# Performance work log

Measured on AMD Instinct MI355X. Metric: run time of the kernel, lower is better.

The kernel has to match this reference:

```python
import jax, jax.numpy as jnp
import numpy as np

N_ROUTES = 200000
N_REGIONS = 2048
D_IN = 3
EMBED_DIM0 = 100
LSTM_DIM = 100
H1 = 1000
D_OUT = 100


def setup_inputs() -> dict:
    key = jax.random.key(0)
    ks = jax.random.split(key, 14)
    s = 0.1
    return {
        "routes_last": jax.random.normal(ks[0], (N_ROUTES, D_IN), jnp.float32),
        "route_region_ids": jax.random.randint(ks[1], (N_ROUTES,), 0, N_REGIONS),
        # linear0: Linear(3, 100)
        "W0": jax.random.normal(ks[2], (EMBED_DIM0, D_IN), jnp.float32) * s,
        "b0": jax.random.normal(ks[3], (EMBED_DIM0,), jnp.float32) * s,
        # LSTMCell(100, 100): gate order i, f, g, o
        "Wih": jax.random.normal(ks[4], (4 * LSTM_DIM, EMBED_DIM0), jnp.float32) * s,
        "bih": jax.random.normal(ks[5], (4 * LSTM_DIM,), jnp.float32) * s,
        "Whh": jax.random.normal(ks[6], (4 * LSTM_DIM, LSTM_DIM), jnp.float32) * s,
        "bhh": jax.random.normal(ks[7], (4 * LSTM_DIM,), jnp.float32) * s,
        # learned initial state (nn.Parameter rand(1, lstm_dim))
        "h0": jax.random.uniform(ks[8], (1, LSTM_DIM), jnp.float32),
        "c0": jax.random.uniform(ks[9], (1, LSTM_DIM), jnp.float32),
        # linears1: Linear(100,1000) -> ReLU -> Linear(1000,100)
        "W1": jax.random.normal(ks[10], (H1, LSTM_DIM), jnp.float32) * s,
        "b1": jax.random.normal(ks[11], (H1,), jnp.float32) * s,
        "W2": jax.random.normal(ks[12], (D_OUT, H1), jnp.float32) * s,
        "b2": jax.random.normal(ks[13], (D_OUT,), jnp.float32) * s,
        "num_regions": N_REGIONS,
    }


def reference(routes_last, route_region_ids, W0, b0, Wih, bih, Whh, bhh, h0, c0, W1, b1, W2, b2, num_regions):
    # Note: the original LSTM loop always restarts from (h0, c0) and keeps only the
    # last hx, so only the last timestep of each route matters. routes_last is that point.
    e = routes_last @ W0.T + b0                       # [N, 100]
    gates = e @ Wih.T + bih + (h0 @ Whh.T + bhh)      # [N, 400]; h0 broadcasts
    i_g, f_g, g_g, o_g = jnp.split(gates, 4, axis=-1)
    c = jax.nn.sigmoid(f_g) * c0 + jax.nn.sigmoid(i_g) * jnp.tanh(g_g)
    h = jax.nn.sigmoid(o_g) * jnp.tanh(c)             # [N, 100]
    hx = jax.nn.relu(h @ W1.T + b1) @ W2.T + b2       # [N, 100]
    # sum routes within each region (ragged sum)
    region_emb = jax.ops.segment_sum(hx, route_region_ids, num_segments=num_regions)  # [R, 100]
    region_emb = region_emb / jnp.linalg.norm(region_emb, axis=-1, keepdims=True)
    cov = region_emb @ region_emb.T                   # [R, R] cosine similarity
    idx = jnp.arange(num_regions)
    cov = cov.at[idx, idx].set(-jnp.inf)
    return cov
```

## Files before the change

### kernel.cpp

```cpp
#include <hip/hip_runtime.h>
#include <math.h>

#define NR 200000
#define NREG 2048
#define BR 128
#define NBLK 1563

typedef short bf16x8 __attribute__((ext_vector_type(8)));
typedef float f32x4 __attribute__((ext_vector_type(4)));

#define SH_WIH 410752
#define SH_W1  (SH_WIH + 57344)
#define SH_W2  (SH_W1 + 131072)
#define B_LIST 1427712
#define B_CNT  2227712
#define B_BASE 2235904
#define B_CURS 2244112
#define B_HXB  2252800
#define WS_REQ 91852800ULL

#define L_SA  0
#define L_HB  16384
#define L_SB  16384
#define L_T1  30720
#define L_XS  49152
#define L_GBP 50688
#define L_C0P 52480
#define L_B1C 52928
#define L_RID 53184
#define L_BYTES 53696

__device__ __forceinline__ unsigned f2bf(float f) {
    unsigned u = __builtin_bit_cast(unsigned, f);
    u += 0x7fff + ((u >> 16) & 1);
    return u >> 16;
}
__device__ __forceinline__ unsigned cvtpk(float lo, float hi) {
    unsigned r;
    asm("v_cvt_pk_bf16_f32 %0, %1, %2" : "=v"(r) : "v"(lo), "v"(hi));
    return r;
}
__device__ __forceinline__ float sigm(float x) { return 1.0f / (1.0f + __expf(-x)); }
__device__ __forceinline__ float tanhfast(float x) {
    float t = __expf(2.0f * fabsf(x));
    float r = 1.0f - 2.0f / (t + 1.0f);
    return copysignf(r, x);
}
__device__ __forceinline__ f32x4 mfma16(bf16x8 a, bf16x8 b, f32x4 c) {
    return __builtin_amdgcn_mfma_f32_16x16x32_bf16(a, b, c, 0, 0, 0);
}

__global__ __launch_bounds__(1024) void k_zero(float* __restrict__ p, int n) {
    int i = blockIdx.x * 1024 + threadIdx.x;
    if (i < n) p[i] = 0.0f;
}

__global__ __launch_bounds__(256) void k_hist(const int* __restrict__ ids,
                                              int* __restrict__ cnt) {
    int i = blockIdx.x * 256 + threadIdx.x;
    if (i < NR) atomicAdd(&cnt[ids[i]], 1);
}

__global__ __launch_bounds__(1024) void k_scan(const int* __restrict__ cnt,
                                               int* __restrict__ base,
                                               int* __restrict__ cursor) {
    __shared__ int sc[2048];
    const int t = threadIdx.x;
    sc[t] = cnt[t];
    sc[t + 1024] = cnt[t + 1024];
    __syncthreads();
    for (int off = 1; off < 2048; off <<= 1) {
        int v0 = (t >= off) ? sc[t - off] : 0;
        int v1 = sc[t + 1024 - off];
        __syncthreads();
        sc[t] += v0;
        sc[t + 1024] += v1;
        __syncthreads();
    }
    int b0 = (t == 0) ? 0 : sc[t - 1];
    int b1v = sc[t + 1023];
    base[t] = b0;          cursor[t] = b0;
    base[t + 1024] = b1v;  cursor[t + 1024] = b1v;
    if (t == 0) base[2048] = sc[2047];
}

__global__ __launch_bounds__(256) void k_scatter(const int* __restrict__ ids,
                                                 int* __restrict__ cursor,
                                                 int* __restrict__ list) {
    int i = blockIdx.x * 256 + threadIdx.x;
    if (i < NR) {
        int pos = atomicAdd(&cursor[ids[i]], 1);
        list[pos] = i;
    }
}

__global__ __launch_bounds__(256) void k_prep(
    const float* __restrict__ Wih, const float* __restrict__ bih,
    const float* __restrict__ bhh, const float* __restrict__ Whh,
    const float* __restrict__ h0,  const float* __restrict__ c0,
    const float* __restrict__ W1,  const float* __restrict__ W2,
    float* __restrict__ wsf, short* __restrict__ wsh)
{
    int idx = blockIdx.x * 256 + threadIdx.x;
    if (idx < 57344) {
        int st = idx >> 13, s = idx & 8191;
        int row = s >> 7, c4 = (s >> 3) & 15, e = s & 7;
        int kc = c4 ^ (row & 15);
        int k = kc * 8 + e;
        int g = row >> 4, j = st * 16 + (row & 15);
        float v = (j < 100 && k < 100) ? Wih[(g * 100 + j) * 100 + k] : 0.f;
        wsh[SH_WIH + idx] = (short)f2bf(v);
        return;
    }
    idx -= 57344;
    if (idx < 131072) {
        int st = idx >> 13, s = idx & 8191;
        int row = s >> 7, c4 = (s >> 3) & 15, e = s & 7;
        int kc = c4 ^ (row & 15);
        int k = kc * 8 + e;
        int m = st * 64 + row;
        float v = (m < 1000 && k < 100) ? W1[m * 100 + k] : 0.f;
        wsh[SH_W1 + idx] = (short)f2bf(v);
        return;
    }
    idx -= 131072;
    if (idx < 114688) {
        int st = idx / 7168, s = idx - st * 7168;
        int row = s >> 6, c4 = (s >> 3) & 7, e = s & 7;
        int kc = c4 ^ (row & 7);
        int m = st * 64 + kc * 8 + e;
        float v = (row < 100 && m < 1000) ? W2[row * 1000 + m] : 0.f;
        wsh[SH_W2 + idx] = (short)f2bf(v);
        return;
    }
    idx -= 114688;
    if (idx < 448) {
        int jt = idx >> 6, r = idx & 63, g = r >> 4, j = jt * 16 + (r & 15);
        float s = 0.f;
        if (j < 100) {
            s = bih[g * 100 + j] + bhh[g * 100 + j];
            const float* wr = &Whh[(g * 100 + j) * 100];
            for (int k = 0; k < 100; ++k) s += h0[k] * wr[k];
        }
        wsf[204800 + idx] = s;
        return;
    }
    idx -= 448;
    if (idx < 112) wsf[205248 + idx] = (idx < 100) ? c0[idx] : 0.f;
}

__global__ __launch_bounds__(256, 3) void k_routes(
    const float* __restrict__ routes, const int* __restrict__ ids,
    const float* __restrict__ W0, const float* __restrict__ b0,
    const float* __restrict__ b1, const float* __restrict__ b2,
    const float* __restrict__ wsf, const short* __restrict__ wsh,
    float* __restrict__ racc, float* __restrict__ hxb, int use_hxb)
{
    __shared__ __align__(16) float ldsf[L_BYTES / 4];
    char* L = (char*)ldsf;
    const int tid = threadIdx.x;
    const int w = tid >> 6, l = tid & 63;
    const int lr = l & 15, lg = l >> 4;
    const int rbase = blockIdx.x * BR;

    float* xs  = (float*)(L + L_XS);
    float* gbp = (float*)(L + L_GBP);
    float* c0p = (float*)(L + L_C0P);
    float* b1c = (float*)(L + L_B1C);
    int*   rid = (int*)(L + L_RID);

    if (tid < 96) {
        float4 v;
        int gi = rbase * 3 + tid * 4;
        v.x = (gi + 0 < NR * 3) ? routes[gi + 0] : 0.f;
        v.y = (gi + 1 < NR * 3) ? routes[gi + 1] : 0.f;
        v.z = (gi + 2 < NR * 3) ? routes[gi + 2] : 0.f;
        v.w = (gi + 3 < NR * 3) ? routes[gi + 3] : 0.f;
        *(float4*)(xs + tid * 4) = v;
    } else if (tid >= 128) {
        int t = tid - 128;
        rid[t] = (rbase + t < NR) ? ids[rbase + t] : 0;
    }
    for (int i = tid; i < 448; i += 256) gbp[i] = wsf[204800 + i];
    for (int i = tid; i < 112; i += 256) c0p[i] = wsf[205248 + i];
    if (tid < 128) {
        int q = tid & 15;
        f32x4 z = {0.f, 0.f, 0.f, 0.f};
        *(f32x4*)(L + L_HB + tid * 256 + ((14 ^ q) << 4)) = z;
        *(f32x4*)(L + L_HB + tid * 256 + ((15 ^ q) << 4)) = z;
    }
    __syncthreads();

    bf16x8 be[2][4];
    #pragma unroll
    for (int rt = 0; rt < 2; ++rt) {
        int rl = w * 32 + rt * 16 + lr;
        float x0 = xs[rl * 3], x1 = xs[rl * 3 + 1], x2 = xs[rl * 3 + 2];
        #pragma unroll
        for (int ks = 0; ks < 4; ++ks) {
            bf16x8 v;
            #pragma unroll
            for (int j = 0; j < 8; ++j) {
                int k = ks * 32 + lg * 8 + j;
                float e = 0.f;
                if (k < 100)
                    e = b0[k] + x0 * W0[3 * k] + x1 * W0[3 * k + 1] + x2 * W0[3 * k + 2];
                v[j] = (short)f2bf(e);
            }
            be[rt][ks] = v;
        }
    }

    const f32x4* gsrc = (const f32x4*)(wsh + SH_WIH);
    f32x4 pa[4];
    #pragma unroll
    for (int t = 0; t < 4; ++t) pa[t] = gsrc[tid + t * 256];
    #pragma unroll 1
    for (int jt = 0; jt < 7; ++jt) {
        __syncthreads();
        {
            f32x4* dst = (f32x4*)(L + L_SA);
            #pragma unroll
            for (int t = 0; t < 4; ++t) dst[tid + t * 256] = pa[t];
        }
        __syncthreads();
        if (jt < 6) {
            #pragma unroll
            for (int t = 0; t < 4; ++t) pa[t] = gsrc[(jt + 1) * 1024 + tid + t * 256];
        }
        f32x4 acc[4][2];
        #pragma unroll
        for (int g = 0; g < 4; ++g) {
            bf16x8 aw[4];
            #pragma unroll
            for (int ks = 0; ks < 4; ++ks)
                aw[ks] = *(bf16x8*)(L + L_SA + (g * 16 + lr) * 256 + (((lg + 4 * ks) ^ lr) << 4));
            #pragma unroll
            for (int rt = 0; rt < 2; ++rt) {
                f32x4 a = {0.f, 0.f, 0.f, 0.f};
                #pragma unroll
                for (int ks = 0; ks < 4; ++ks) a = mfma16(aw[ks], be[rt][ks], a);
                acc[g][rt] = a;
            }
        }
        const f32x4 gi_ = *(const f32x4*)(gbp + jt * 64 +  0 + lg * 4);
        const f32x4 gf_ = *(const f32x4*)(gbp + jt * 64 + 16 + lg * 4);
        const f32x4 gg_ = *(const f32x4*)(gbp + jt * 64 + 32 + lg * 4);
        const f32x4 go_ = *(const f32x4*)(gbp + jt * 64 + 48 + lg * 4);
        const f32x4 c0v = *(const f32x4*)(c0p + jt * 16 + lg * 4);
        #pragma unroll
        for (int rt = 0; rt < 2; ++rt) {
            int route = w * 32 + rt * 16 + lr;
            float hv[4];
            #pragma unroll
            for (int i = 0; i < 4; ++i) {
                float iv = sigm(acc[0][rt][i] + gi_[i]);
                float fv = sigm(acc[1][rt][i] + gf_[i]);
                float gv = tanhfast(acc[2][rt][i] + gg_[i]);
                float ov = sigm(acc[3][rt][i] + go_[i]);
                float c  = fv * c0v[i] + iv * gv;
                hv[i] = ov * tanhfast(c);
            }
            uint2 hu;
            hu.x = cvtpk(hv[0], hv[1]);
            hu.y = cvtpk(hv[2], hv[3]);
            int c4 = 2 * jt + (lg >> 1);
            *(uint2*)(L + L_HB + route * 256 + ((c4 ^ lr) << 4) + (lg & 1) * 8) = hu;
        }
    }

    bf16x8 bh[2][4];
    #pragma unroll
    for (int rt = 0; rt < 2; ++rt)
        #pragma unroll
        for (int ks = 0; ks < 4; ++ks)
            bh[rt][ks] = *(bf16x8*)(L + L_HB + (w * 32 + rt * 16 + lr) * 256 + (((lg + 4 * ks) ^ lr) << 4));

    const f32x4* s1 = (const f32x4*)(wsh + SH_W1);
    const f32x4* s2 = (const f32x4*)(wsh + SH_W2);
    f32x4 p1[4], p2[4];
    float pb1 = 0.f;
    #pragma unroll
    for (int t = 0; t < 4; ++t) p1[t] = s1[tid + t * 256];
    #pragma unroll
    for (int t = 0; t < 4; ++t) {
        int s = tid + t * 256;
        p2[t] = (s < 896) ? s2[s] : f32x4{0.f, 0.f, 0.f, 0.f};
    }
    if (tid < 64) pb1 = b1[tid];

    f32x4 hx[7][2] = {};
    #pragma unroll 1
    for (int mc = 0; mc < 16; ++mc) {
        __syncthreads();
        {
            f32x4* d1 = (f32x4*)(L + L_SA);
            #pragma unroll
            for (int t = 0; t < 4; ++t) d1[tid + t * 256] = p1[t];
            f32x4* d2 = (f32x4*)(L + L_SB);
            #pragma unroll
            for (int t = 0; t < 4; ++t) {
                int s = tid + t * 256;
                if (s < 896) d2[s] = p2[t];
            }
            if (tid < 64) b1c[tid] = pb1;
        }
        __syncthreads();
        if (mc < 15) {
            #pragma unroll
            for (int t = 0; t < 4; ++t) p1[t] = s1[(mc + 1) * 1024 + tid + t * 256];
            #pragma unroll
            for (int t = 0; t < 4; ++t) {
                int s = tid + t * 256;
                if (s < 896) p2[t] = s2[(mc + 1) * 896 + s];
            }
            if (tid < 64) {
                int m = (mc + 1) * 64 + tid;
                pb1 = (m < 1000) ? b1[m] : 0.f;
            }
        }
        #pragma unroll
        for (int mt = 0; mt < 4; ++mt) {
            bf16x8 aw[4];
            #pragma unroll
            for (int ks = 0; ks < 4; ++ks)
                aw[ks] = *(bf16x8*)(L + L_SA + (mt * 16 + lr) * 256 + (((lg + 4 * ks) ^ lr) << 4));
            const f32x4 b1v = *(const f32x4*)(b1c + mt * 16 + lg * 4);
            #pragma unroll
            for (int rt = 0; rt < 2; ++rt) {
                f32x4 a = {0.f, 0.f, 0.f, 0.f};
                #pragma unroll
                for (int ks = 0; ks < 4; ++ks) a = mfma16(aw[ks], bh[rt][ks], a);
                int route = w * 32 + rt * 16 + lr;
                uint2 tu;
                tu.x = cvtpk(fmaxf(a[0] + b1v[0], 0.f), fmaxf(a[1] + b1v[1], 0.f));
                tu.y = cvtpk(fmaxf(a[2] + b1v[2], 0.f), fmaxf(a[3] + b1v[3], 0.f));
                int c4 = 2 * mt + (lg >> 1);
                *(uint2*)(L + L_T1 + route * 128 + ((c4 ^ (lr & 7)) << 4) + (lg & 1) * 8) = tu;
            }
        }
        bf16x8 bt[2][2];
        #pragma unroll
        for (int rt = 0; rt < 2; ++rt)
            #pragma unroll
            for (int k2 = 0; k2 < 2; ++k2)
                bt[rt][k2] = *(bf16x8*)(L + L_T1 + (w * 32 + rt * 16 + lr) * 128 + (((4 * k2 + lg) ^ (lr & 7)) << 4));
        #pragma unroll
        for (int dt = 0; dt < 7; ++dt) {
            bf16x8 aw2[2];
            #pragma unroll
            for (int k2 = 0; k2 < 2; ++k2)
                aw2[k2] = *(bf16x8*)(L + L_SB + (dt * 16 + lr) * 128 + (((4 * k2 + lg) ^ (lr & 7)) << 4));
            #pragma unroll
            for (int rt = 0; rt < 2; ++rt)
                #pragma unroll
                for (int k2 = 0; k2 < 2; ++k2)
                    hx[dt][rt] = mfma16(aw2[k2], bt[rt][k2], hx[dt][rt]);
        }
    }

    if (use_hxb) {
        #pragma unroll
        for (int rt = 0; rt < 2; ++rt) {
            int rl = w * 32 + rt * 16 + lr;
            if (rbase + rl < NR) {
                float* dst = hxb + (rbase + rl) * 112;
                #pragma unroll
                for (int dt = 0; dt < 7; ++dt) {
                    int d0 = dt * 16 + lg * 4;
                    f32x4 v = hx[dt][rt];
                    #pragma unroll
                    for (int i = 0; i < 4; ++i)
                        v[i] += (d0 + i < 100) ? b2[d0 + i] : 0.f;
                    *(f32x4*)(dst + d0) = v;
                }
            }
        }
    } else {
        #pragma unroll
        for (int rt = 0; rt < 2; ++rt) {
            int rl = w * 32 + rt * 16 + lr;
            if (rbase + rl < NR) {
                float* dst = &racc[rid[rl] * 100];
                #pragma unroll
                for (int dt = 0; dt < 7; ++dt) {
                    int dbase = dt * 16 + lg * 4;
                    #pragma unroll
                    for (int i = 0; i < 4; ++i) {
                        int d = dbase + i;
                        if (d < 100) atomicAdd(&dst[d], hx[dt][rt][i] + b2[d]);
                    }
                }
            }
        }
    }
}

__global__ __launch_bounds__(128) void k_segsum(const int* __restrict__ base,
                                                const int* __restrict__ list,
                                                const float* __restrict__ hxb,
                                                float* __restrict__ racc) {
    __shared__ int ll[1024];
    __shared__ float pp[2];
    const int reg = blockIdx.x, t = threadIdx.x;
    const int s = base[reg], e = base[reg + 1];
    const int n = e - s;
    const int d = t;
    float acc = 0.f;
    if (n <= 1024) {
        for (int i = t; i < n; i += 128) ll[i] = list[s + i];
        __syncthreads();
        #pragma unroll 2
        for (int i = 0; i < n; ++i) {
            int rt = ll[i];
            if (d < 112) acc += hxb[rt * 112 + d];
        }
    } else {
        for (int i = 0; i < n; ++i) {
            int rt = list[s + i];
            if (d < 112) acc += hxb[rt * 112 + d];
        }
    }
    float sq = (d < 100) ? acc * acc : 0.f;
    #pragma unroll
    for (int o = 32; o; o >>= 1) sq += __shfl_xor(sq, o);
    if ((t & 63) == 0) pp[t >> 6] = sq;
    __syncthreads();
    float rn = 1.0f / sqrtf(pp[0] + pp[1]);
    if (d < 100) racc[reg * 100 + d] = acc * rn;
}

__global__ __launch_bounds__(64) void k_norm(float* __restrict__ E) {
    const int r = blockIdx.x;
    const int l = threadIdx.x;
    float v0 = E[r * 100 + l];
    float v1 = (l < 36) ? E[r * 100 + 64 + l] : 0.0f;
    float s = v0 * v0 + v1 * v1;
    #pragma unroll
    for (int o = 32; o; o >>= 1) s += __shfl_xor(s, o);
    const float rn = 1.0f / sqrtf(s);
    E[r * 100 + l] = v0 * rn;
    if (l < 36) E[r * 100 + 64 + l] = v1 * rn;
}

#define ST 68
__global__ __launch_bounds__(256) void k_cov(const float* __restrict__ E,
                                             float* __restrict__ out) {
    __shared__ float aT[100 * ST];
    __shared__ float bT[100 * ST];
    const int bi = blockIdx.x, bj = blockIdx.y;
    const int tid = threadIdx.x;
    for (int idx = tid; idx < 6400; idx += 256) {
        int ii = idx / 100, k = idx - ii * 100;
        aT[k * ST + ii] = E[(bi * 64 + ii) * 100 + k];
        bT[k * ST + ii] = E[(bj * 64 + ii) * 100 + k];
    }
    __syncthreads();
    const int rg = tid >> 4, jg = tid & 15;
    const int r0 = rg * 4, c0 = jg * 4;
    float acc[4][4] = {};
    #pragma unroll 4
    for (int k = 0; k < 100; ++k) {
        const float4 a = *(const float4*)&aT[k * ST + r0];
        const float4 b = *(const float4*)&bT[k * ST + c0];
        const float ar[4] = {a.x, a.y, a.z, a.w};
        const float br[4] = {b.x, b.y, b.z, b.w};
        #pragma unroll
        for (int i = 0; i < 4; ++i)
            #pragma unroll
            for (int jj = 0; jj < 4; ++jj)
                acc[i][jj] += ar[i] * br[jj];
    }
    const float dsent = -3.0e38f;
    #pragma unroll
    for (int i = 0; i < 4; ++i) {
        const int row = bi * 64 + r0 + i;
        const int colb = bj * 64 + c0;
        float4 v;
        v.x = (row == colb + 0) ? dsent : acc[i][0];
        v.y = (row == colb + 1) ? dsent : acc[i][1];
        v.z = (row == colb + 2) ? dsent : acc[i][2];
        v.w = (row == colb + 3) ? dsent : acc[i][3];
        *(float4*)&out[row * 2048 + colb] = v;
    }
}

extern "C" void kernel_launch(void* const* d_in, const int* in_sizes, int n_in,
                              void* d_out, int out_size, void* d_ws, size_t ws_size,
                              hipStream_t stream) {
    (void)in_sizes; (void)n_in; (void)out_size;
    const float* routes = (const float*)d_in[0];
    const int*   ids    = (const int*)d_in[1];
    const float* W0  = (const float*)d_in[2];
    const float* b0  = (const float*)d_in[3];
    const float* Wih = (const float*)d_in[4];
    const float* bih = (const float*)d_in[5];
    const float* Whh = (const float*)d_in[6];
    const float* bhh = (const float*)d_in[7];
    const float* h0  = (const float*)d_in[8];
    const float* c0  = (const float*)d_in[9];
    const float* W1  = (const float*)d_in[10];
    const float* b1  = (const float*)d_in[11];
    const float* W2  = (const float*)d_in[12];
    const float* b2  = (const float*)d_in[13];
    float* out  = (float*)d_out;
    float* wsf  = (float*)d_ws;
    short* wsh  = (short*)d_ws;
    char*  wsb  = (char*)d_ws;
    float* racc = wsf;
    int*   list = (int*)(wsb + B_LIST);
    int*   cnt  = (int*)(wsb + B_CNT);
    int*   base = (int*)(wsb + B_BASE);
    int*   curs = (int*)(wsb + B_CURS);
    float* hxb  = (float*)(wsb + B_HXB);

    const bool fast = (ws_size >= WS_REQ);

    hipLaunchKernelGGL(k_prep, dim3(1187), dim3(256), 0, stream,
                       Wih, bih, bhh, Whh, h0, c0, W1, W2, wsf, wsh);
    if (fast) {
        hipLaunchKernelGGL(k_zero, dim3(2), dim3(1024), 0, stream, (float*)cnt, 2048);
        hipLaunchKernelGGL(k_hist, dim3(782), dim3(256), 0, stream, ids, cnt);
        hipLaunchKernelGGL(k_scan, dim3(1), dim3(1024), 0, stream, cnt, base, curs);
        hipLaunchKernelGGL(k_scatter, dim3(782), dim3(256), 0, stream, ids, curs, list);
        hipLaunchKernelGGL(k_routes, dim3(NBLK), dim3(256), 0, stream,
                           routes, ids, W0, b0, b1, b2, wsf, wsh, racc, hxb, 1);
        hipLaunchKernelGGL(k_segsum, dim3(NREG), dim3(128), 0, stream,
                           base, list, hxb, racc);
    } else {
        hipLaunchKernelGGL(k_zero, dim3(200), dim3(1024), 0, stream, racc, 204800);
        hipLaunchKernelGGL(k_routes, dim3(NBLK), dim3(256), 0, stream,
                           routes, ids, W0, b0, b1, b2, wsf, wsh, racc, hxb, 0);
        hipLaunchKernelGGL(k_norm, dim3(NREG), dim3(64), 0, stream, racc);
    }
    hipLaunchKernelGGL(k_cov, dim3(32, 32), dim3(256), 0, stream, racc, out);
}
```

Measured before the change: 406.3 us.

## Scatter route outputs in bf16 to region-sorted slots; fuse prep with histogram

The route kernel now writes each hx row as bf16 straight to its region-sorted slot, using a position array from the scatter pass. The segment-sum kernel can then read contiguous rows with 8 groups of threads instead of gathering through an index list, and the intermediate buffer is half as large. W2 fragments are loaded from global memory directly into registers rather than staged through LDS. The histogram is merged into the prep kernel and the zeroing kernel is replaced by a memset, cutting launches. Storing hx in bf16 loses some precision in the sums, and the route kernel's stores become scattered.

```diff
diff --git a/kernel.cpp b/kernel.cpp
--- a/kernel.cpp
+++ b/kernel.cpp
@@ -12,16 +12,15 @@
 #define SH_WIH 410752
 #define SH_W1  (SH_WIH + 57344)
 #define SH_W2  (SH_W1 + 131072)
-#define B_LIST 1427712
+#define B_POS  1427712
 #define B_CNT  2227712
 #define B_BASE 2235904
 #define B_CURS 2244112
 #define B_HXB  2252800
-#define WS_REQ 91852800ULL
+#define WS_REQ 47052800ULL
 
 #define L_SA  0
 #define L_HB  16384
-#define L_SB  16384
 #define L_T1  30720
 #define L_XS  49152
 #define L_GBP 50688
@@ -40,6 +39,12 @@
     asm("v_cvt_pk_bf16_f32 %0, %1, %2" : "=v"(r) : "v"(lo), "v"(hi));
     return r;
 }
+__device__ __forceinline__ float bf2f_lo(unsigned u) {
+    return __builtin_bit_cast(float, u << 16);
+}
+__device__ __forceinline__ float bf2f_hi(unsigned u) {
+    return __builtin_bit_cast(float, u & 0xffff0000u);
+}
 __device__ __forceinline__ float sigm(float x) { return 1.0f / (1.0f + __expf(-x)); }
 __device__ __forceinline__ float tanhfast(float x) {
     float t = __expf(2.0f * fabsf(x));
@@ -53,12 +58,6 @@
 __global__ __launch_bounds__(1024) void k_zero(float* __restrict__ p, int n) {
     int i = blockIdx.x * 1024 + threadIdx.x;
     if (i < n) p[i] = 0.0f;
-}
-
-__global__ __launch_bounds__(256) void k_hist(const int* __restrict__ ids,
-                                              int* __restrict__ cnt) {
-    int i = blockIdx.x * 256 + threadIdx.x;
-    if (i < NR) atomicAdd(&cnt[ids[i]], 1);
 }
 
 __global__ __launch_bounds__(1024) void k_scan(const int* __restrict__ cnt,
@@ -86,21 +85,24 @@
 
 __global__ __launch_bounds__(256) void k_scatter(const int* __restrict__ ids,
                                                  int* __restrict__ cursor,
-                                                 int* __restrict__ list) {
+                                                 int* __restrict__ pos) {
     int i = blockIdx.x * 256 + threadIdx.x;
-    if (i < NR) {
-        int pos = atomicAdd(&cursor[ids[i]], 1);
-        list[pos] = i;
-    }
-}
-
-__global__ __launch_bounds__(256) void k_prep(
+    if (i < NR) pos[i] = atomicAdd(&cursor[ids[i]], 1);
+}
+
+__global__ __launch_bounds__(256) void k_prephist(
     const float* __restrict__ Wih, const float* __restrict__ bih,
     const float* __restrict__ bhh, const float* __restrict__ Whh,
     const float* __restrict__ h0,  const float* __restrict__ c0,
     const float* __restrict__ W1,  const float* __restrict__ W2,
-    float* __restrict__ wsf, short* __restrict__ wsh)
+    float* __restrict__ wsf, short* __restrict__ wsh,
+    const int* __restrict__ ids, int* __restrict__ cnt, int nprep)
 {
+    if ((int)blockIdx.x >= nprep) {
+        int i = (blockIdx.x - nprep) * 256 + threadIdx.x;
+        if (i < NR) atomicAdd(&cnt[ids[i]], 1);
+        return;
+    }
     int idx = blockIdx.x * 256 + threadIdx.x;
     if (idx < 57344) {
         int st = idx >> 13, s = idx & 8191;
@@ -154,7 +156,8 @@
     const float* __restrict__ W0, const float* __restrict__ b0,
     const float* __restrict__ b1, const float* __restrict__ b2,
     const float* __restrict__ wsf, const short* __restrict__ wsh,
-    float* __restrict__ racc, float* __restrict__ hxb, int use_hxb)
+    float* __restrict__ racc, unsigned short* __restrict__ hxb,
+    const int* __restrict__ pos, int use_hxb)
 {
     __shared__ __align__(16) float ldsf[L_BYTES / 4];
     char* L = (char*)ldsf;
@@ -179,7 +182,8 @@
         *(float4*)(xs + tid * 4) = v;
     } else if (tid >= 128) {
         int t = tid - 128;
-        rid[t] = (rbase + t < NR) ? ids[rbase + t] : 0;
+        int g = rbase + t;
+        rid[t] = (g < NR) ? (use_hxb ? pos[g] : ids[g]) : 0;
     }
     for (int i = tid; i < 448; i += 256) gbp[i] = wsf[204800 + i];
     for (int i = tid; i < 112; i += 256) c0p[i] = wsf[205248 + i];
@@ -277,16 +281,11 @@
             bh[rt][ks] = *(bf16x8*)(L + L_HB + (w * 32 + rt * 16 + lr) * 256 + (((lg + 4 * ks) ^ lr) << 4));
 
     const f32x4* s1 = (const f32x4*)(wsh + SH_W1);
-    const f32x4* s2 = (const f32x4*)(wsh + SH_W2);
-    f32x4 p1[4], p2[4];
+    const char*  w2img = (const char*)(wsh + SH_W2);
+    f32x4 p1[4];
     float pb1 = 0.f;
     #pragma unroll
     for (int t = 0; t < 4; ++t) p1[t] = s1[tid + t * 256];
-    #pragma unroll
-    for (int t = 0; t < 4; ++t) {
-        int s = tid + t * 256;
-        p2[t] = (s < 896) ? s2[s] : f32x4{0.f, 0.f, 0.f, 0.f};
-    }
     if (tid < 64) pb1 = b1[tid];
 
     f32x4 hx[7][2] = {};
@@ -297,23 +296,19 @@
             f32x4* d1 = (f32x4*)(L + L_SA);
             #pragma unroll
             for (int t = 0; t < 4; ++t) d1[tid + t * 256] = p1[t];
-            f32x4* d2 = (f32x4*)(L + L_SB);
-            #pragma unroll
-            for (int t = 0; t < 4; ++t) {
-                int s = tid + t * 256;
-                if (s < 896) d2[s] = p2[t];
-            }
             if (tid < 64) b1c[tid] = pb1;
         }
         __syncthreads();
+        const char* w2b = w2img + mc * 14336 + (lr * 128);
+        bf16x8 aw2a[7], aw2b[7];
+        #pragma unroll
+        for (int dt = 0; dt < 7; ++dt) {
+            aw2a[dt] = *(const bf16x8*)(w2b + dt * 2048 + ((lg ^ (lr & 7)) << 4));
+            aw2b[dt] = *(const bf16x8*)(w2b + dt * 2048 + (((4 + lg) ^ (lr & 7)) << 4));
+        }
         if (mc < 15) {
             #pragma unroll
             for (int t = 0; t < 4; ++t) p1[t] = s1[(mc + 1) * 1024 + tid + t * 256];
-            #pragma unroll
-            for (int t = 0; t < 4; ++t) {
-                int s = tid + t * 256;
-                if (s < 896) p2[t] = s2[(mc + 1) * 896 + s];
-            }
             if (tid < 64) {
                 int m = (mc + 1) * 64 + tid;
                 pb1 = (m < 1000) ? b1[m] : 0.f;
@@ -346,17 +341,15 @@
             for (int k2 = 0; k2 < 2; ++k2)
                 bt[rt][k2] = *(bf16x8*)(L + L_T1 + (w * 32 + rt * 16 + lr) * 128 + (((4 * k2 + lg) ^ (lr & 7)) << 4));
         #pragma unroll
-        for (int dt = 0; dt < 7; ++dt) {
-            bf16x8 aw2[2];
-            #pragma unroll
-            for (int k2 = 0; k2 < 2; ++k2)
-                aw2[k2] = *(bf16x8*)(L + L_SB + (dt * 16 + lr) * 128 + (((4 * k2 + lg) ^ (lr & 7)) << 4));
+        for (int dt = 0; dt < 7; ++dt)
             #pragma unroll
             for (int rt = 0; rt < 2; ++rt)
-                #pragma unroll
-                for (int k2 = 0; k2 < 2; ++k2)
-                    hx[dt][rt] = mfma16(aw2[k2], bt[rt][k2], hx[dt][rt]);
-        }
+                hx[dt][rt] = mfma16(aw2a[dt], bt[rt][0], hx[dt][rt]);
+        #pragma unroll
+        for (int dt = 0; dt < 7; ++dt)
+            #pragma unroll
+            for (int rt = 0; rt < 2; ++rt)
+                hx[dt][rt] = mfma16(aw2b[dt], bt[rt][1], hx[dt][rt]);
     }
 
     if (use_hxb) {
@@ -364,15 +357,18 @@
         for (int rt = 0; rt < 2; ++rt) {
             int rl = w * 32 + rt * 16 + lr;
             if (rbase + rl < NR) {
-                float* dst = hxb + (rbase + rl) * 112;
+                unsigned short* dst = hxb + (size_t)rid[rl] * 112;
                 #pragma unroll
                 for (int dt = 0; dt < 7; ++dt) {
                     int d0 = dt * 16 + lg * 4;
-                    f32x4 v = hx[dt][rt];
-                    #pragma unroll
-                    for (int i = 0; i < 4; ++i)
-                        v[i] += (d0 + i < 100) ? b2[d0 + i] : 0.f;
-                    *(f32x4*)(dst + d0) = v;
+                    float v0 = hx[dt][rt][0] + ((d0 + 0 < 100) ? b2[d0 + 0] : 0.f);
+                    float v1 = hx[dt][rt][1] + ((d0 + 1 < 100) ? b2[d0 + 1] : 0.f);
+                    float v2 = hx[dt][rt][2] + ((d0 + 2 < 100) ? b2[d0 + 2] : 0.f);
+                    float v3 = hx[dt][rt][3] + ((d0 + 3 < 100) ? b2[d0 + 3] : 0.f);
+                    uint2 u;
+                    u.x = cvtpk(v0, v1);
+                    u.y = cvtpk(v2, v3);
+                    *(uint2*)(dst + d0) = u;
                 }
             }
         }
@@ -396,38 +392,41 @@
     }
 }
 
-__global__ __launch_bounds__(128) void k_segsum(const int* __restrict__ base,
-                                                const int* __restrict__ list,
-                                                const float* __restrict__ hxb,
+__global__ __launch_bounds__(256) void k_segsum(const int* __restrict__ base,
+                                                const unsigned short* __restrict__ hxb,
                                                 float* __restrict__ racc) {
-    __shared__ int ll[1024];
+    __shared__ float red[8][116];
     __shared__ float pp[2];
     const int reg = blockIdx.x, t = threadIdx.x;
-    const int s = base[reg], e = base[reg + 1];
-    const int n = e - s;
-    const int d = t;
-    float acc = 0.f;
-    if (n <= 1024) {
-        for (int i = t; i < n; i += 128) ll[i] = list[s + i];
-        __syncthreads();
-        #pragma unroll 2
-        for (int i = 0; i < n; ++i) {
-            int rt = ll[i];
-            if (d < 112) acc += hxb[rt * 112 + d];
-        }
-    } else {
-        for (int i = 0; i < n; ++i) {
-            int rt = list[s + i];
-            if (d < 112) acc += hxb[rt * 112 + d];
-        }
-    }
-    float sq = (d < 100) ? acc * acc : 0.f;
-    #pragma unroll
-    for (int o = 32; o; o >>= 1) sq += __shfl_xor(sq, o);
-    if ((t & 63) == 0) pp[t >> 6] = sq;
+    const int s = base[reg];
+    const int n = base[reg + 1] - s;
+    const int grp = t >> 5, cl = t & 31;
+    f32x4 acc = {0.f, 0.f, 0.f, 0.f};
+    if (cl < 28) {
+        for (int i = grp; i < n; i += 8) {
+            uint2 u = *(const uint2*)(hxb + (size_t)(s + i) * 112 + cl * 4);
+            acc[0] += bf2f_lo(u.x); acc[1] += bf2f_hi(u.x);
+            acc[2] += bf2f_lo(u.y); acc[3] += bf2f_hi(u.y);
+        }
+        *(f32x4*)&red[grp][cl * 4] = acc;
+    }
     __syncthreads();
-    float rn = 1.0f / sqrtf(pp[0] + pp[1]);
-    if (d < 100) racc[reg * 100 + d] = acc * rn;
+    float v = 0.f, sq = 0.f;
+    if (t < 128) {
+        if (t < 112) {
+            #pragma unroll
+            for (int g = 0; g < 8; ++g) v += red[g][t];
+        }
+        sq = (t < 100) ? v * v : 0.f;
+        #pragma unroll
+        for (int o = 32; o; o >>= 1) sq += __shfl_xor(sq, o);
+        if ((t & 63) == 0) pp[t >> 6] = sq;
+    }
+    __syncthreads();
+    if (t < 100) {
+        float rn = 1.0f / sqrtf(pp[0] + pp[1]);
+        racc[reg * 100 + t] = v * rn;
+    }
 }
 
 __global__ __launch_bounds__(64) void k_norm(float* __restrict__ E) {
@@ -508,29 +507,30 @@
     short* wsh  = (short*)d_ws;
     char*  wsb  = (char*)d_ws;
     float* racc = wsf;
-    int*   list = (int*)(wsb + B_LIST);
+    int*   pos  = (int*)(wsb + B_POS);
     int*   cnt  = (int*)(wsb + B_CNT);
     int*   base = (int*)(wsb + B_BASE);
     int*   curs = (int*)(wsb + B_CURS);
-    float* hxb  = (float*)(wsb + B_HXB);
+    unsigned short* hxb = (unsigned short*)(wsb + B_HXB);
 
     const bool fast = (ws_size >= WS_REQ);
 
-    hipLaunchKernelGGL(k_prep, dim3(1187), dim3(256), 0, stream,
-                       Wih, bih, bhh, Whh, h0, c0, W1, W2, wsf, wsh);
     if (fast) {
-        hipLaunchKernelGGL(k_zero, dim3(2), dim3(1024), 0, stream, (float*)cnt, 2048);
-        hipLaunchKernelGGL(k_hist, dim3(782), dim3(256), 0, stream, ids, cnt);
+        hipMemsetAsync(cnt, 0, 2048 * sizeof(int), stream);
+        hipLaunchKernelGGL(k_prephist, dim3(1969), dim3(256), 0, stream,
+                           Wih, bih, bhh, Whh, h0, c0, W1, W2, wsf, wsh, ids, cnt, 1187);
         hipLaunchKernelGGL(k_scan, dim3(1), dim3(1024), 0, stream, cnt, base, curs);
-        hipLaunchKernelGGL(k_scatter, dim3(782), dim3(256), 0, stream, ids, curs, list);
+        hipLaunchKernelGGL(k_scatter, dim3(782), dim3(256), 0, stream, ids, curs, pos);
         hipLaunchKernelGGL(k_routes, dim3(NBLK), dim3(256), 0, stream,
-                           routes, ids, W0, b0, b1, b2, wsf, wsh, racc, hxb, 1);
-        hipLaunchKernelGGL(k_segsum, dim3(NREG), dim3(128), 0, stream,
-                           base, list, hxb, racc);
+                           routes, ids, W0, b0, b1, b2, wsf, wsh, racc, hxb, pos, 1);
+        hipLaunchKernelGGL(k_segsum, dim3(NREG), dim3(256), 0, stream,
+                           base, hxb, racc);
     } else {
+        hipLaunchKernelGGL(k_prephist, dim3(1187), dim3(256), 0, stream,
+                           Wih, bih, bhh, Whh, h0, c0, W1, W2, wsf, wsh, ids, cnt, 1187);
         hipLaunchKernelGGL(k_zero, dim3(200), dim3(1024), 0, stream, racc, 204800);
         hipLaunchKernelGGL(k_routes, dim3(NBLK), dim3(256), 0, stream,
-                           routes, ids, W0, b0, b1, b2, wsf, wsh, racc, hxb, 0);
+                           routes, ids, W0, b0, b1, b2, wsf, wsh, racc, hxb, pos, 0);
         hipLaunchKernelGGL(k_norm, dim3(NREG), dim3(64), 0, stream, racc);
     }
     hipLaunchKernelGGL(k_cov, dim3(32, 32), dim3(256), 0, stream, racc, out);
```

Result: slower. 624.2 us (+53.6%).
